# Kernel tuning notes

Measured on AMD Instinct MI355X. Metric: run time of the kernel, lower is better.

Reference implementation:

```python
import jax, jax.numpy as jnp
from jax import lax
import numpy as np

VOCAB, EMB, SEQ, HID, BATCH = 50000, 300, 80, 128, 4096


def setup_inputs() -> dict:
    key = jax.random.key(0)
    ks = jax.random.split(key, 7)
    x = jax.random.randint(ks[0], (BATCH, SEQ), 0, VOCAB)
    emb = jax.random.normal(ks[1], (VOCAB, EMB), jnp.float32) * 0.05  # frozen pretrained table
    # Keras SimpleRNN: kernel (glorot), recurrent_kernel (orthogonal-ish), bias zeros
    Wxh = jax.random.normal(ks[2], (EMB, HID), jnp.float32) * (1.0 / np.sqrt(EMB))
    Whh = jax.random.normal(ks[3], (HID, HID), jnp.float32) * (1.0 / np.sqrt(HID))
    bh = jnp.zeros((HID,), jnp.float32)
    Wd = jax.random.normal(ks[4], (HID, 1), jnp.float32) * (1.0 / np.sqrt(HID))
    bd = jnp.zeros((1,), jnp.float32)
    return {"x": x, "emb": emb, "Wxh": Wxh, "Whh": Whh, "bh": bh, "Wd": Wd, "bd": bd}


def reference(x, emb, Wxh, Whh, bh, Wd, bd):
    # Embedding lookup: [B, T] -> [B, T, E]
    e = emb[x]
    # Precompute input projection for all timesteps: [B, T, H]
    xp = jnp.einsum('bte,eh->bth', e, Wxh) + bh
    # SimpleRNN recurrence (tanh), return only last hidden state
    def step(h, xt):  # xt: [B, H]
        h = jnp.tanh(xt + h @ Whh)
        return h, None
    h0 = jnp.zeros((x.shape[0], Whh.shape[0]), xp.dtype)
    h_last, _ = lax.scan(step, h0, jnp.swapaxes(xp, 0, 1))  # scan over time
    # Dense(1, sigmoid): [B, 1]
    return jax.nn.sigmoid(h_last @ Wd + bd)
```

## Files before the change

### kernel.cpp

```cpp
#include <hip/hip_runtime.h>
#include <hip/hip_fp16.h>
#include <cstdint>

#define VOCAB 50000
#define EMB   300
#define SEQ   80
#define HID   128
#define BATCH 4096

typedef __attribute__((ext_vector_type(8))) _Float16 f16x8;
typedef __attribute__((ext_vector_type(4))) float    f32x4;

static __device__ __forceinline__ float fast_tanh(float xv) {
    const float e = __expf(2.f * xv);
    float r;
    asm("v_rcp_f32 %0, %1" : "=v"(r) : "v"(e + 1.f));
    return fmaf(-2.f, r, 1.f);
}
static __device__ __forceinline__ float f16b2f(unsigned short u) {
    _Float16 h; __builtin_memcpy(&h, &u, 2); return (float)h;
}
static __device__ __forceinline__ unsigned pack2h(float a, float b) {
    _Float16 ha = (_Float16)a, hb = (_Float16)b;
    unsigned short ua, ub;
    __builtin_memcpy(&ua, &ha, 2); __builtin_memcpy(&ub, &hb, 2);
    return (unsigned)ua | ((unsigned)ub << 16);
}

__global__ __launch_bounds__(256) void k_wprep(const float* __restrict__ Wxh,
                                               _Float16* __restrict__ W2) {
    const int c = blockIdx.x * 256 + threadIdx.x;
    if (c >= 5120) return;
    const int ks = c >> 9, rem = c & 511, col = rem >> 2, g = rem & 3;
    f16x8 f;
    #pragma unroll
    for (int j = 0; j < 8; ++j) {
        const int k = 32 * ks + 8 * g + j;
        f[j] = (_Float16)(k < EMB ? Wxh[k * HID + col] : 0.f);
    }
    *reinterpret_cast<f16x8*>(W2 + (size_t)c * 8) = f;
}

__global__ __launch_bounds__(256) void k_ptab(
    const float*    __restrict__ emb,
    const _Float16* __restrict__ W2,
    const float*    __restrict__ bh,
    _Float16*       __restrict__ P)
{
    __shared__ __align__(16) unsigned char Ps[16 * 256];

    const int tid = threadIdx.x, lane = tid & 63, wv = tid >> 6;
    const int r16 = lane & 15, g = lane >> 4;
    const int v0 = blockIdx.x * 64;

    f16x8 wa[10], wb[10];
    #pragma unroll
    for (int ks = 0; ks < 10; ++ks) {
        const int colA = 32 * wv + r16;
        wa[ks] = *reinterpret_cast<const f16x8*>(W2 + ((size_t)ks * 512 + colA * 4 + g) * 8);
        wb[ks] = *reinterpret_cast<const f16x8*>(W2 + ((size_t)ks * 512 + (colA + 16) * 4 + g) * 8);
    }
    const float4 bhA = *reinterpret_cast<const float4*>(bh + 32 * wv + 4 * g);
    const float4 bhB = *reinterpret_cast<const float4*>(bh + 32 * wv + 16 + 4 * g);

    const int psA = r16 * 256 + (((4 * wv + (g >> 1)) ^ r16) & 15) * 16 + (g & 1) * 8;
    const int psB = r16 * 256 + (((4 * wv + 2 + (g >> 1)) ^ r16) & 15) * 16 + (g & 1) * 8;
    const int srow = tid >> 4, schunk = tid & 15;
    const int sbyte = srow * 256 + ((schunk ^ srow) & 15) * 16;

    for (int tile = 0; tile < 4; ++tile) {
        const int row = v0 + tile * 16 + r16;
        const float* rp = emb + (size_t)min(row, VOCAB - 1) * EMB;

        f32x4 accA = {0.f, 0.f, 0.f, 0.f}, accB = {0.f, 0.f, 0.f, 0.f};
        #pragma unroll
        for (int ks = 0; ks < 9; ++ks) {
            const int c0 = 32 * ks + 8 * g;
            const float4 u0 = *reinterpret_cast<const float4*>(rp + c0);
            const float4 u1 = *reinterpret_cast<const float4*>(rp + c0 + 4);
            f16x8 ef;
            ef[0]=(_Float16)u0.x; ef[1]=(_Float16)u0.y; ef[2]=(_Float16)u0.z; ef[3]=(_Float16)u0.w;
            ef[4]=(_Float16)u1.x; ef[5]=(_Float16)u1.y; ef[6]=(_Float16)u1.z; ef[7]=(_Float16)u1.w;
            accA = __builtin_amdgcn_mfma_f32_16x16x32_f16(wa[ks], ef, accA, 0, 0, 0);
            accB = __builtin_amdgcn_mfma_f32_16x16x32_f16(wb[ks], ef, accB, 0, 0, 0);
        }
        {
            f16x8 ef;
            #pragma unroll
            for (int j = 0; j < 8; ++j) ef[j] = (_Float16)0.f;
            if (g == 0) {
                const float4 u0 = *reinterpret_cast<const float4*>(rp + 288);
                const float4 u1 = *reinterpret_cast<const float4*>(rp + 292);
                ef[0]=(_Float16)u0.x; ef[1]=(_Float16)u0.y; ef[2]=(_Float16)u0.z; ef[3]=(_Float16)u0.w;
                ef[4]=(_Float16)u1.x; ef[5]=(_Float16)u1.y; ef[6]=(_Float16)u1.z; ef[7]=(_Float16)u1.w;
            } else if (g == 1) {
                const float4 u0 = *reinterpret_cast<const float4*>(rp + 296);
                ef[0]=(_Float16)u0.x; ef[1]=(_Float16)u0.y; ef[2]=(_Float16)u0.z; ef[3]=(_Float16)u0.w;
            }
            accA = __builtin_amdgcn_mfma_f32_16x16x32_f16(wa[9], ef, accA, 0, 0, 0);
            accB = __builtin_amdgcn_mfma_f32_16x16x32_f16(wb[9], ef, accB, 0, 0, 0);
        }

        uint2 oA, oB;
        oA.x = pack2h(accA[0] + bhA.x, accA[1] + bhA.y);
        oA.y = pack2h(accA[2] + bhA.z, accA[3] + bhA.w);
        oB.x = pack2h(accB[0] + bhB.x, accB[1] + bhB.y);
        oB.y = pack2h(accB[2] + bhB.z, accB[3] + bhB.w);
        *reinterpret_cast<uint2*>(&Ps[psA]) = oA;
        *reinterpret_cast<uint2*>(&Ps[psB]) = oB;
        __syncthreads();

        const int orow = v0 + tile * 16 + srow;
        if (orow < VOCAB)
            *reinterpret_cast<uint4*>(P + (size_t)orow * HID + schunk * 8) =
                *reinterpret_cast<const uint4*>(&Ps[sbyte]);
        __syncthreads();
    }
}

__global__ __launch_bounds__(512, 2) void k_rnn(
    const int*      __restrict__ x,
    const _Float16* __restrict__ P,
    const float*    __restrict__ Whh,
    const float*    __restrict__ Wd,
    const float*    __restrict__ bd,
    float*          __restrict__ out)
{
    __shared__ __align__(16) unsigned char Xb[2][16 * 256];
    __shared__ __align__(16) unsigned char Hb[2][16 * 256];
    __shared__ int xidx[16 * SEQ];

    const int tid = threadIdx.x, lane = tid & 63, wv = tid >> 6;
    const int r16 = lane & 15, g = lane >> 4;
    const int rb = blockIdx.x * 16;

    for (int q = tid; q < 16 * SEQ; q += 512) xidx[q] = x[rb * SEQ + q];
    if (tid < 256) { uint4 z = {}; *reinterpret_cast<uint4*>(&Hb[0][tid * 16]) = z; }

    const int col = 16 * wv + r16;

    int h_rd[4];
    #pragma unroll
    for (int ks = 0; ks < 4; ++ks)
        h_rd[ks] = r16 * 256 + (((4 * ks + g) ^ r16) & 15) * 16;
    const int hw = r16 * 256 + (((2 * wv + (g >> 1)) ^ r16) & 15) * 16 + (g & 1) * 8;

    f16x8 wh[4];
    #pragma unroll
    for (int ks = 0; ks < 4; ++ks) {
        f16x8 f;
        #pragma unroll
        for (int j = 0; j < 8; ++j)
            f[j] = (_Float16)Whh[(32 * ks + 8 * g + j) * HID + col];
        wh[ks] = f;
    }

    const bool gon  = (tid < 256);
    const int  grow = (tid >> 4) & 15, gk = tid & 15;
    const int  gdst = grow * 256 + ((gk ^ grow) & 15) * 16;

    __syncthreads();

    if (gon)
        *reinterpret_cast<uint4*>(&Xb[0][gdst]) = *reinterpret_cast<const uint4*>(
            P + (size_t)xidx[grow * SEQ] * HID + 8 * gk);
    uint4 cur = {}, nxt = {};
    if (gon) cur = *reinterpret_cast<const uint4*>(
        P + (size_t)xidx[grow * SEQ + 1] * HID + 8 * gk);

    asm volatile("s_waitcnt lgkmcnt(0)" ::: "memory");
    __builtin_amdgcn_s_barrier();
    __builtin_amdgcn_sched_barrier(0);

#define STEP(T, PB, CUR, NXT)                                                      \
    {                                                                              \
        if ((T) + 1 < SEQ && gon)                                                  \
            *reinterpret_cast<uint4*>(&Xb[(PB) ^ 1][gdst]) = CUR;                  \
        if ((T) + 2 < SEQ && gon)                                                  \
            NXT = *reinterpret_cast<const uint4*>(                                 \
                P + (size_t)xidx[grow * SEQ + (T) + 2] * HID + 8 * gk);            \
        const uint2 xv = *reinterpret_cast<const uint2*>(&Xb[PB][hw]);             \
        f32x4 accA, accB = {0.f, 0.f, 0.f, 0.f};                                   \
        accA[0] = f16b2f((unsigned short)(xv.x & 0xffff));                         \
        accA[1] = f16b2f((unsigned short)(xv.x >> 16));                            \
        accA[2] = f16b2f((unsigned short)(xv.y & 0xffff));                         \
        accA[3] = f16b2f((unsigned short)(xv.y >> 16));                            \
        const f16x8 h0 = *reinterpret_cast<const f16x8*>(&Hb[PB][h_rd[0]]);        \
        const f16x8 h1 = *reinterpret_cast<const f16x8*>(&Hb[PB][h_rd[1]]);        \
        const f16x8 h2 = *reinterpret_cast<const f16x8*>(&Hb[PB][h_rd[2]]);        \
        const f16x8 h3 = *reinterpret_cast<const f16x8*>(&Hb[PB][h_rd[3]]);        \
        accA = __builtin_amdgcn_mfma_f32_16x16x32_f16(wh[0], h0, accA, 0, 0, 0);   \
        accB = __builtin_amdgcn_mfma_f32_16x16x32_f16(wh[1], h1, accB, 0, 0, 0);   \
        accA = __builtin_amdgcn_mfma_f32_16x16x32_f16(wh[2], h2, accA, 0, 0, 0);   \
        accB = __builtin_amdgcn_mfma_f32_16x16x32_f16(wh[3], h3, accB, 0, 0, 0);   \
        uint2 hv;                                                                  \
        hv.x = pack2h(fast_tanh(accA[0] + accB[0]), fast_tanh(accA[1] + accB[1])); \
        hv.y = pack2h(fast_tanh(accA[2] + accB[2]), fast_tanh(accA[3] + accB[3])); \
        *reinterpret_cast<uint2*>(&Hb[(PB) ^ 1][hw]) = hv;                         \
        asm volatile("s_waitcnt lgkmcnt(0)" ::: "memory");                         \
        __builtin_amdgcn_s_barrier();                                              \
        __builtin_amdgcn_sched_barrier(0);                                         \
    }

    for (int t = 0; t < SEQ; t += 2) {
        STEP(t,     0, cur, nxt);
        STEP(t + 1, 1, nxt, cur);
    }
#undef STEP

    const int r = tid >> 5, m = tid & 31;
    const int fb = r * 256 + (((m >> 1) ^ r) & 15) * 16 + (m & 1) * 8;
    const uint2 hv = *reinterpret_cast<const uint2*>(&Hb[0][fb]);
    const float4 wd = *reinterpret_cast<const float4*>(&Wd[4 * m]);
    float part = f16b2f((unsigned short)(hv.x & 0xffff)) * wd.x
               + f16b2f((unsigned short)(hv.x >> 16))    * wd.y
               + f16b2f((unsigned short)(hv.y & 0xffff)) * wd.z
               + f16b2f((unsigned short)(hv.y >> 16))    * wd.w;
    part += __shfl_down(part, 16, 32);
    part += __shfl_down(part, 8, 32);
    part += __shfl_down(part, 4, 32);
    part += __shfl_down(part, 2, 32);
    part += __shfl_down(part, 1, 32);
    if (m == 0) out[rb + r] = 1.f / (1.f + expf(-(part + bd[0])));
}

extern "C" void kernel_launch(void* const* d_in, const int* in_sizes, int n_in,
                              void* d_out, int out_size, void* d_ws, size_t ws_size,
                              hipStream_t stream)
{
    (void)in_sizes; (void)n_in; (void)out_size; (void)ws_size;
    const int*   x   = (const int*)  d_in[0];
    const float* emb = (const float*)d_in[1];
    const float* Wxh = (const float*)d_in[2];
    const float* Whh = (const float*)d_in[3];
    const float* bh  = (const float*)d_in[4];
    const float* Wd  = (const float*)d_in[5];
    const float* bd  = (const float*)d_in[6];
    float* out = (float*)d_out;

    _Float16* P  = (_Float16*)d_ws;
    _Float16* W2 = (_Float16*)((char*)d_ws + 12800000);

    k_wprep<<<20, 256, 0, stream>>>(Wxh, W2);
    k_ptab<<<(VOCAB + 63) / 64, 256, 0, stream>>>(emb, W2, bh, P);
    k_rnn<<<BATCH / 16, 512, 0, stream>>>(x, P, Whh, Wd, bd, out);
}
```

Measured before the change: 72.02 us.

## Halve RNN block rows, drop LDS x-staging, prefetch next embedding tile in ptab

The recurrence kernel now gives each 256-thread block 8 batch rows instead of 16, and each wave computes 32 hidden columns with two MFMA accumulators. This doubles the grid, aiming to fill more CUs and give each block shorter per-step work. The projected input is loaded straight from global memory into registers, one step ahead, instead of being staged through an LDS buffer. This removes the LDS write and read per step. The padded MFMA rows 8-15 duplicate row 7, so half the MFMA work is wasted. The projection-table kernel also software-pipelines its embedding-row loads one tile ahead, at the cost of more registers.

```diff
diff --git a/kernel.cpp b/kernel.cpp
--- a/kernel.cpp
+++ b/kernel.cpp
@@ -41,7 +41,7 @@
     *reinterpret_cast<f16x8*>(W2 + (size_t)c * 8) = f;
 }
 
-__global__ __launch_bounds__(256) void k_ptab(
+__global__ __launch_bounds__(256, 2) void k_ptab(
     const float*    __restrict__ emb,
     const _Float16* __restrict__ W2,
     const float*    __restrict__ bh,
@@ -68,37 +68,43 @@
     const int srow = tid >> 4, schunk = tid & 15;
     const int sbyte = srow * 256 + ((schunk ^ srow) & 15) * 16;
 
+    float4 u0[10], u1[10];
+
+#define LOADT(TILE)                                                               \
+    {                                                                             \
+        const float* rp = emb + (size_t)min(v0 + (TILE) * 16 + r16, VOCAB - 1) * EMB; \
+        _Pragma("unroll")                                                         \
+        for (int ks = 0; ks < 9; ++ks) {                                          \
+            u0[ks] = *reinterpret_cast<const float4*>(rp + 32 * ks + 8 * g);      \
+            u1[ks] = *reinterpret_cast<const float4*>(rp + 32 * ks + 8 * g + 4);  \
+        }                                                                         \
+        float4 z = {0.f, 0.f, 0.f, 0.f};                                          \
+        u0[9] = (g == 0) ? *reinterpret_cast<const float4*>(rp + 288)             \
+              : (g == 1) ? *reinterpret_cast<const float4*>(rp + 296) : z;        \
+        u1[9] = (g == 0) ? *reinterpret_cast<const float4*>(rp + 292) : z;        \
+    }
+
+    LOADT(0)
+
+    #pragma unroll
     for (int tile = 0; tile < 4; ++tile) {
-        const int row = v0 + tile * 16 + r16;
-        const float* rp = emb + (size_t)min(row, VOCAB - 1) * EMB;
+        f16x8 ef[10];
+        #pragma unroll
+        for (int ks = 0; ks < 10; ++ks) {
+            f16x8 f;
+            f[0] = (_Float16)u0[ks].x; f[1] = (_Float16)u0[ks].y;
+            f[2] = (_Float16)u0[ks].z; f[3] = (_Float16)u0[ks].w;
+            f[4] = (_Float16)u1[ks].x; f[5] = (_Float16)u1[ks].y;
+            f[6] = (_Float16)u1[ks].z; f[7] = (_Float16)u1[ks].w;
+            ef[ks] = f;
+        }
+        if (tile < 3) LOADT(tile + 1)
 
         f32x4 accA = {0.f, 0.f, 0.f, 0.f}, accB = {0.f, 0.f, 0.f, 0.f};
         #pragma unroll
-        for (int ks = 0; ks < 9; ++ks) {
-            const int c0 = 32 * ks + 8 * g;
-            const float4 u0 = *reinterpret_cast<const float4*>(rp + c0);
-            const float4 u1 = *reinterpret_cast<const float4*>(rp + c0 + 4);
-            f16x8 ef;
-            ef[0]=(_Float16)u0.x; ef[1]=(_Float16)u0.y; ef[2]=(_Float16)u0.z; ef[3]=(_Float16)u0.w;
-            ef[4]=(_Float16)u1.x; ef[5]=(_Float16)u1.y; ef[6]=(_Float16)u1.z; ef[7]=(_Float16)u1.w;
-            accA = __builtin_amdgcn_mfma_f32_16x16x32_f16(wa[ks], ef, accA, 0, 0, 0);
-            accB = __builtin_amdgcn_mfma_f32_16x16x32_f16(wb[ks], ef, accB, 0, 0, 0);
-        }
-        {
-            f16x8 ef;
-            #pragma unroll
-            for (int j = 0; j < 8; ++j) ef[j] = (_Float16)0.f;
-            if (g == 0) {
-                const float4 u0 = *reinterpret_cast<const float4*>(rp + 288);
-                const float4 u1 = *reinterpret_cast<const float4*>(rp + 292);
-                ef[0]=(_Float16)u0.x; ef[1]=(_Float16)u0.y; ef[2]=(_Float16)u0.z; ef[3]=(_Float16)u0.w;
-                ef[4]=(_Float16)u1.x; ef[5]=(_Float16)u1.y; ef[6]=(_Float16)u1.z; ef[7]=(_Float16)u1.w;
-            } else if (g == 1) {
-                const float4 u0 = *reinterpret_cast<const float4*>(rp + 296);
-                ef[0]=(_Float16)u0.x; ef[1]=(_Float16)u0.y; ef[2]=(_Float16)u0.z; ef[3]=(_Float16)u0.w;
-            }
-            accA = __builtin_amdgcn_mfma_f32_16x16x32_f16(wa[9], ef, accA, 0, 0, 0);
-            accB = __builtin_amdgcn_mfma_f32_16x16x32_f16(wb[9], ef, accB, 0, 0, 0);
+        for (int ks = 0; ks < 10; ++ks) {
+            accA = __builtin_amdgcn_mfma_f32_16x16x32_f16(wa[ks], ef[ks], accA, 0, 0, 0);
+            accB = __builtin_amdgcn_mfma_f32_16x16x32_f16(wb[ks], ef[ks], accB, 0, 0, 0);
         }
 
         uint2 oA, oB;
@@ -116,9 +122,10 @@
                 *reinterpret_cast<const uint4*>(&Ps[sbyte]);
         __syncthreads();
     }
-}
-
-__global__ __launch_bounds__(512, 2) void k_rnn(
+#undef LOADT
+}
+
+__global__ __launch_bounds__(256, 2) void k_rnn(
     const int*      __restrict__ x,
     const _Float16* __restrict__ P,
     const float*    __restrict__ Whh,
@@ -126,91 +133,107 @@
     const float*    __restrict__ bd,
     float*          __restrict__ out)
 {
-    __shared__ __align__(16) unsigned char Xb[2][16 * 256];
     __shared__ __align__(16) unsigned char Hb[2][16 * 256];
-    __shared__ int xidx[16 * SEQ];
+    __shared__ int xidx[8 * SEQ];
 
     const int tid = threadIdx.x, lane = tid & 63, wv = tid >> 6;
     const int r16 = lane & 15, g = lane >> 4;
-    const int rb = blockIdx.x * 16;
-
-    for (int q = tid; q < 16 * SEQ; q += 512) xidx[q] = x[rb * SEQ + q];
-    if (tid < 256) { uint4 z = {}; *reinterpret_cast<uint4*>(&Hb[0][tid * 16]) = z; }
-
-    const int col = 16 * wv + r16;
+    const int rb = blockIdx.x * 8;
+    const int r8 = min(r16, 7);
+
+    for (int q = tid; q < 8 * SEQ; q += 256) xidx[q] = x[rb * SEQ + q];
+    for (int q = tid; q < 512; q += 256) {
+        uint4 z = {};
+        *reinterpret_cast<uint4*>(&Hb[0][0] + 0) = z;
+        reinterpret_cast<uint4*>(&Hb[0][0])[q] = z;
+    }
+
+    const int cA = 32 * wv + 4 * g;
 
     int h_rd[4];
     #pragma unroll
     for (int ks = 0; ks < 4; ++ks)
         h_rd[ks] = r16 * 256 + (((4 * ks + g) ^ r16) & 15) * 16;
-    const int hw = r16 * 256 + (((2 * wv + (g >> 1)) ^ r16) & 15) * 16 + (g & 1) * 8;
-
-    f16x8 wh[4];
+    const int hw0 = r16 * 256 + (((4 * wv + (g >> 1)) ^ r16) & 15) * 16 + (g & 1) * 8;
+    const int hw1 = r16 * 256 + (((4 * wv + 2 + (g >> 1)) ^ r16) & 15) * 16 + (g & 1) * 8;
+
+    f16x8 wh0[4], wh1[4];
     #pragma unroll
     for (int ks = 0; ks < 4; ++ks) {
-        f16x8 f;
+        f16x8 f0, f1;
         #pragma unroll
-        for (int j = 0; j < 8; ++j)
-            f[j] = (_Float16)Whh[(32 * ks + 8 * g + j) * HID + col];
-        wh[ks] = f;
-    }
-
-    const bool gon  = (tid < 256);
-    const int  grow = (tid >> 4) & 15, gk = tid & 15;
-    const int  gdst = grow * 256 + ((gk ^ grow) & 15) * 16;
+        for (int j = 0; j < 8; ++j) {
+            const int k = 32 * ks + 8 * g + j;
+            f0[j] = (_Float16)Whh[k * HID + 32 * wv + r16];
+            f1[j] = (_Float16)Whh[k * HID + 32 * wv + 16 + r16];
+        }
+        wh0[ks] = f0; wh1[ks] = f1;
+    }
 
     __syncthreads();
 
-    if (gon)
-        *reinterpret_cast<uint4*>(&Xb[0][gdst]) = *reinterpret_cast<const uint4*>(
-            P + (size_t)xidx[grow * SEQ] * HID + 8 * gk);
-    uint4 cur = {}, nxt = {};
-    if (gon) cur = *reinterpret_cast<const uint4*>(
-        P + (size_t)xidx[grow * SEQ + 1] * HID + 8 * gk);
-
-    asm volatile("s_waitcnt lgkmcnt(0)" ::: "memory");
-    __builtin_amdgcn_s_barrier();
-    __builtin_amdgcn_sched_barrier(0);
-
-#define STEP(T, PB, CUR, NXT)                                                      \
+    uint2 xa0, xa1, xb0, xb1;
+    {
+        const _Float16* p0 = P + (size_t)xidx[r8 * SEQ + 0] * HID + cA;
+        xa0 = *reinterpret_cast<const uint2*>(p0);
+        xa1 = *reinterpret_cast<const uint2*>(p0 + 16);
+        const _Float16* p1 = P + (size_t)xidx[r8 * SEQ + 1] * HID + cA;
+        xb0 = *reinterpret_cast<const uint2*>(p1);
+        xb1 = *reinterpret_cast<const uint2*>(p1 + 16);
+    }
+
+#define STEP(T, PB, CA0, CA1)                                                      \
     {                                                                              \
-        if ((T) + 1 < SEQ && gon)                                                  \
-            *reinterpret_cast<uint4*>(&Xb[(PB) ^ 1][gdst]) = CUR;                  \
-        if ((T) + 2 < SEQ && gon)                                                  \
-            NXT = *reinterpret_cast<const uint4*>(                                 \
-                P + (size_t)xidx[grow * SEQ + (T) + 2] * HID + 8 * gk);            \
-        const uint2 xv = *reinterpret_cast<const uint2*>(&Xb[PB][hw]);             \
-        f32x4 accA, accB = {0.f, 0.f, 0.f, 0.f};                                   \
-        accA[0] = f16b2f((unsigned short)(xv.x & 0xffff));                         \
-        accA[1] = f16b2f((unsigned short)(xv.x >> 16));                            \
-        accA[2] = f16b2f((unsigned short)(xv.y & 0xffff));                         \
-        accA[3] = f16b2f((unsigned short)(xv.y >> 16));                            \
-        const f16x8 h0 = *reinterpret_cast<const f16x8*>(&Hb[PB][h_rd[0]]);        \
-        const f16x8 h1 = *reinterpret_cast<const f16x8*>(&Hb[PB][h_rd[1]]);        \
-        const f16x8 h2 = *reinterpret_cast<const f16x8*>(&Hb[PB][h_rd[2]]);        \
-        const f16x8 h3 = *reinterpret_cast<const f16x8*>(&Hb[PB][h_rd[3]]);        \
-        accA = __builtin_amdgcn_mfma_f32_16x16x32_f16(wh[0], h0, accA, 0, 0, 0);   \
-        accB = __builtin_amdgcn_mfma_f32_16x16x32_f16(wh[1], h1, accB, 0, 0, 0);   \
-        accA = __builtin_amdgcn_mfma_f32_16x16x32_f16(wh[2], h2, accA, 0, 0, 0);   \
-        accB = __builtin_amdgcn_mfma_f32_16x16x32_f16(wh[3], h3, accB, 0, 0, 0);   \
-        uint2 hv;                                                                  \
-        hv.x = pack2h(fast_tanh(accA[0] + accB[0]), fast_tanh(accA[1] + accB[1])); \
-        hv.y = pack2h(fast_tanh(accA[2] + accB[2]), fast_tanh(accA[3] + accB[3])); \
-        *reinterpret_cast<uint2*>(&Hb[(PB) ^ 1][hw]) = hv;                         \
+        f32x4 accA, accB;                                                          \
+        accA[0] = f16b2f((unsigned short)(CA0.x & 0xffff));                        \
+        accA[1] = f16b2f((unsigned short)(CA0.x >> 16));                           \
+        accA[2] = f16b2f((unsigned short)(CA0.y & 0xffff));                        \
+        accA[3] = f16b2f((unsigned short)(CA0.y >> 16));                           \
+        accB[0] = f16b2f((unsigned short)(CA1.x & 0xffff));                        \
+        accB[1] = f16b2f((unsigned short)(CA1.x >> 16));                           \
+        accB[2] = f16b2f((unsigned short)(CA1.y & 0xffff));                        \
+        accB[3] = f16b2f((unsigned short)(CA1.y >> 16));                           \
+        if ((T) + 2 < SEQ) {                 \
+            const _Float16* np = P + (size_t)xidx[r8 * SEQ + (T) + 2] * HID + cA;  \
+            CA0 = *reinterpret_cast<const uint2*>(np);                             \
+            CA1 = *reinterpret_cast<const uint2*>(np + 16);                        \
+        }                                                                          \
+        const unsigned char* hb = &Hb[PB][0];                                      \
+        const f16x8 h0 = *reinterpret_cast<const f16x8*>(hb + h_rd[0]);            \
+        const f16x8 h1 = *reinterpret_cast<const f16x8*>(hb + h_rd[1]);            \
+        const f16x8 h2 = *reinterpret_cast<const f16x8*>(hb + h_rd[2]);            \
+        const f16x8 h3 = *reinterpret_cast<const f16x8*>(hb + h_rd[3]);            \
+        accA = __builtin_amdgcn_mfma_f32_16x16x32_f16(wh0[0], h0, accA, 0, 0, 0);  \
+        accB = __builtin_amdgcn_mfma_f32_16x16x32_f16(wh1[0], h0, accB, 0, 0, 0);  \
+        accA = __builtin_amdgcn_mfma_f32_16x16x32_f16(wh0[1], h1, accA, 0, 0, 0);  \
+        accB = __builtin_amdgcn_mfma_f32_16x16x32_f16(wh1[1], h1, accB, 0, 0, 0);  \
+        accA = __builtin_amdgcn_mfma_f32_16x16x32_f16(wh0[2], h2, accA, 0, 0, 0);  \
+        accB = __builtin_amdgcn_mfma_f32_16x16x32_f16(wh1[2], h2, accB, 0, 0, 0);  \
+        accA = __builtin_amdgcn_mfma_f32_16x16x32_f16(wh0[3], h3, accA, 0, 0, 0);  \
+        accB = __builtin_amdgcn_mfma_f32_16x16x32_f16(wh1[3], h3, accB, 0, 0, 0);  \
+        unsigned char* hwp = &Hb[(PB) ^ 1][0];                                     \
+        uint2 o0, o1;                                                              \
+        o0.x = pack2h(fast_tanh(accA[0]), fast_tanh(accA[1]));                     \
+        o0.y = pack2h(fast_tanh(accA[2]), fast_tanh(accA[3]));                     \
+        o1.x = pack2h(fast_tanh(accB[0]), fast_tanh(accB[1]));                     \
+        o1.y = pack2h(fast_tanh(accB[2]), fast_tanh(accB[3]));                     \
+        *reinterpret_cast<uint2*>(hwp + hw0) = o0;                                 \
+        *reinterpret_cast<uint2*>(hwp + hw1) = o1;                                 \
         asm volatile("s_waitcnt lgkmcnt(0)" ::: "memory");                         \
         __builtin_amdgcn_s_barrier();                                              \
         __builtin_amdgcn_sched_barrier(0);                                         \
     }
 
     for (int t = 0; t < SEQ; t += 2) {
-        STEP(t,     0, cur, nxt);
-        STEP(t + 1, 1, nxt, cur);
+        STEP(t,     0, xa0, xa1);
+        STEP(t + 1, 1, xb0, xb1);
     }
 #undef STEP
 
+    const char* hb0 = (const char*)&Hb[0][0];
     const int r = tid >> 5, m = tid & 31;
     const int fb = r * 256 + (((m >> 1) ^ r) & 15) * 16 + (m & 1) * 8;
-    const uint2 hv = *reinterpret_cast<const uint2*>(&Hb[0][fb]);
+    const uint2 hv = *reinterpret_cast<const uint2*>(hb0 + fb);
     const float4 wd = *reinterpret_cast<const float4*>(&Wd[4 * m]);
     float part = f16b2f((unsigned short)(hv.x & 0xffff)) * wd.x
                + f16b2f((unsigned short)(hv.x >> 16))    * wd.y
@@ -243,5 +266,5 @@
 
     k_wprep<<<20, 256, 0, stream>>>(Wxh, W2);
     k_ptab<<<(VOCAB + 63) / 64, 256, 0, stream>>>(emb, W2, bh, P);
-    k_rnn<<<BATCH / 16, 512, 0, stream>>>(x, P, Whh, Wd, bd, out);
-}
+    k_rnn<<<BATCH / 8, 256, 0, stream>>>(x, P, Whh, Wd, bd, out);
+}
```

After: 83.99 us. 1.17x slower.

## Run each RNN batch tile in a single wavefront, removing block barriers

Applied to the files above, without the earlier changes.

The recurrence kernel now gives each 16-row batch tile to one 64-lane wavefront. That wavefront holds all of Whh, pre-swizzled by the prep kernel, in registers and computes all 128 hidden columns with 32 MFMAs per step, so the per-step block barrier is gone. The hidden state is exchanged through LDS within the wave only, and the next x-projection rows are gathered straight into registers two steps ahead. The projection-table kernel also changes: each wave handles its own 16 vocab rows, keeps the embedding fragments in registers, streams weight columns through double-buffered registers and writes directly without LDS staging. In exchange, fewer waves run per CU (256 single-wave blocks) and register pressure is high, so parallelism and latency hiding may suffer.

```diff
diff --git a/kernel.cpp b/kernel.cpp
--- a/kernel.cpp
+++ b/kernel.cpp
@@ -28,200 +28,227 @@
 }
 
 __global__ __launch_bounds__(256) void k_wprep(const float* __restrict__ Wxh,
-                                               _Float16* __restrict__ W2) {
+                                               const float* __restrict__ Whh,
+                                               _Float16* __restrict__ W2,
+                                               _Float16* __restrict__ W3) {
     const int c = blockIdx.x * 256 + threadIdx.x;
-    if (c >= 5120) return;
-    const int ks = c >> 9, rem = c & 511, col = rem >> 2, g = rem & 3;
-    f16x8 f;
-    #pragma unroll
-    for (int j = 0; j < 8; ++j) {
-        const int k = 32 * ks + 8 * g + j;
-        f[j] = (_Float16)(k < EMB ? Wxh[k * HID + col] : 0.f);
-    }
-    *reinterpret_cast<f16x8*>(W2 + (size_t)c * 8) = f;
-}
-
-__global__ __launch_bounds__(256) void k_ptab(
+    if (c < 5120) {
+        const int ks = c >> 9, rem = c & 511, col = rem >> 2, g = rem & 3;
+        f16x8 f;
+        #pragma unroll
+        for (int j = 0; j < 8; ++j) {
+            const int k = 32 * ks + 8 * g + j;
+            f[j] = (_Float16)(k < EMB ? Wxh[k * HID + col] : 0.f);
+        }
+        *reinterpret_cast<f16x8*>(W2 + (size_t)c * 8) = f;
+    } else if (c < 7168) {
+        const int c2 = c - 5120;
+        const int ct = c2 >> 8, ks = (c2 >> 6) & 3, l = c2 & 63;
+        const int g = l >> 4, r16 = l & 15;
+        f16x8 f;
+        #pragma unroll
+        for (int j = 0; j < 8; ++j)
+            f[j] = (_Float16)Whh[(32 * ks + 8 * g + j) * HID + 16 * ct + r16];
+        *reinterpret_cast<f16x8*>(W3 + (size_t)c2 * 8) = f;
+    }
+}
+
+__global__ __launch_bounds__(256, 2) void k_ptab(
     const float*    __restrict__ emb,
     const _Float16* __restrict__ W2,
     const float*    __restrict__ bh,
     _Float16*       __restrict__ P)
 {
-    __shared__ __align__(16) unsigned char Ps[16 * 256];
-
     const int tid = threadIdx.x, lane = tid & 63, wv = tid >> 6;
     const int r16 = lane & 15, g = lane >> 4;
-    const int v0 = blockIdx.x * 64;
-
-    f16x8 wa[10], wb[10];
-    #pragma unroll
-    for (int ks = 0; ks < 10; ++ks) {
-        const int colA = 32 * wv + r16;
-        wa[ks] = *reinterpret_cast<const f16x8*>(W2 + ((size_t)ks * 512 + colA * 4 + g) * 8);
-        wb[ks] = *reinterpret_cast<const f16x8*>(W2 + ((size_t)ks * 512 + (colA + 16) * 4 + g) * 8);
-    }
-    const float4 bhA = *reinterpret_cast<const float4*>(bh + 32 * wv + 4 * g);
-    const float4 bhB = *reinterpret_cast<const float4*>(bh + 32 * wv + 16 + 4 * g);
-
-    const int psA = r16 * 256 + (((4 * wv + (g >> 1)) ^ r16) & 15) * 16 + (g & 1) * 8;
-    const int psB = r16 * 256 + (((4 * wv + 2 + (g >> 1)) ^ r16) & 15) * 16 + (g & 1) * 8;
-    const int srow = tid >> 4, schunk = tid & 15;
-    const int sbyte = srow * 256 + ((schunk ^ srow) & 15) * 16;
-
-    for (int tile = 0; tile < 4; ++tile) {
-        const int row = v0 + tile * 16 + r16;
-        const float* rp = emb + (size_t)min(row, VOCAB - 1) * EMB;
-
-        f32x4 accA = {0.f, 0.f, 0.f, 0.f}, accB = {0.f, 0.f, 0.f, 0.f};
-        #pragma unroll
-        for (int ks = 0; ks < 9; ++ks) {
-            const int c0 = 32 * ks + 8 * g;
-            const float4 u0 = *reinterpret_cast<const float4*>(rp + c0);
-            const float4 u1 = *reinterpret_cast<const float4*>(rp + c0 + 4);
-            f16x8 ef;
-            ef[0]=(_Float16)u0.x; ef[1]=(_Float16)u0.y; ef[2]=(_Float16)u0.z; ef[3]=(_Float16)u0.w;
-            ef[4]=(_Float16)u1.x; ef[5]=(_Float16)u1.y; ef[6]=(_Float16)u1.z; ef[7]=(_Float16)u1.w;
-            accA = __builtin_amdgcn_mfma_f32_16x16x32_f16(wa[ks], ef, accA, 0, 0, 0);
-            accB = __builtin_amdgcn_mfma_f32_16x16x32_f16(wb[ks], ef, accB, 0, 0, 0);
-        }
-        {
-            f16x8 ef;
+    const int row = blockIdx.x * 64 + wv * 16 + r16;
+    const float* rp = emb + (size_t)(row < VOCAB ? row : VOCAB - 1) * EMB;
+    const bool wr = (row < VOCAB);
+
+    f16x8 ef[10];
+    #pragma unroll
+    for (int ks = 0; ks < 9; ++ks) {
+        const float4 u0 = *reinterpret_cast<const float4*>(rp + 32 * ks + 8 * g);
+        const float4 u1 = *reinterpret_cast<const float4*>(rp + 32 * ks + 8 * g + 4);
+        f16x8 f;
+        f[0] = (_Float16)u0.x; f[1] = (_Float16)u0.y;
+        f[2] = (_Float16)u0.z; f[3] = (_Float16)u0.w;
+        f[4] = (_Float16)u1.x; f[5] = (_Float16)u1.y;
+        f[6] = (_Float16)u1.z; f[7] = (_Float16)u1.w;
+        ef[ks] = f;
+    }
+    {
+        f16x8 f;
+        #pragma unroll
+        for (int j = 0; j < 8; ++j) f[j] = (_Float16)0.f;
+        if (g == 0) {
+            const float4 u0 = *reinterpret_cast<const float4*>(rp + 288);
+            const float4 u1 = *reinterpret_cast<const float4*>(rp + 292);
+            f[0] = (_Float16)u0.x; f[1] = (_Float16)u0.y;
+            f[2] = (_Float16)u0.z; f[3] = (_Float16)u0.w;
+            f[4] = (_Float16)u1.x; f[5] = (_Float16)u1.y;
+            f[6] = (_Float16)u1.z; f[7] = (_Float16)u1.w;
+        } else if (g == 1) {
+            const float4 u0 = *reinterpret_cast<const float4*>(rp + 296);
+            f[0] = (_Float16)u0.x; f[1] = (_Float16)u0.y;
+            f[2] = (_Float16)u0.z; f[3] = (_Float16)u0.w;
+        }
+        ef[9] = f;
+    }
+
+    float4 bhf[8];
+    #pragma unroll
+    for (int ct = 0; ct < 8; ++ct)
+        bhf[ct] = *reinterpret_cast<const float4*>(bh + 16 * ct + 4 * g);
+
+    f16x8 wA[10], wB[10];
+    #pragma unroll
+    for (int ks = 0; ks < 10; ++ks)
+        wA[ks] = *reinterpret_cast<const f16x8*>(
+            W2 + ((size_t)ks * 512 + (size_t)r16 * 4 + g) * 8);
+
+    char* const po = (char*)(P + (size_t)(wr ? row : 0) * HID);
+
+    #pragma unroll
+    for (int ct = 0; ct < 8; ++ct) {
+        if (ct < 7) {
+            const int coln = 16 * (ct + 1) + r16;
             #pragma unroll
-            for (int j = 0; j < 8; ++j) ef[j] = (_Float16)0.f;
-            if (g == 0) {
-                const float4 u0 = *reinterpret_cast<const float4*>(rp + 288);
-                const float4 u1 = *reinterpret_cast<const float4*>(rp + 292);
-                ef[0]=(_Float16)u0.x; ef[1]=(_Float16)u0.y; ef[2]=(_Float16)u0.z; ef[3]=(_Float16)u0.w;
-                ef[4]=(_Float16)u1.x; ef[5]=(_Float16)u1.y; ef[6]=(_Float16)u1.z; ef[7]=(_Float16)u1.w;
-            } else if (g == 1) {
-                const float4 u0 = *reinterpret_cast<const float4*>(rp + 296);
-                ef[0]=(_Float16)u0.x; ef[1]=(_Float16)u0.y; ef[2]=(_Float16)u0.z; ef[3]=(_Float16)u0.w;
-            }
-            accA = __builtin_amdgcn_mfma_f32_16x16x32_f16(wa[9], ef, accA, 0, 0, 0);
-            accB = __builtin_amdgcn_mfma_f32_16x16x32_f16(wb[9], ef, accB, 0, 0, 0);
-        }
-
-        uint2 oA, oB;
-        oA.x = pack2h(accA[0] + bhA.x, accA[1] + bhA.y);
-        oA.y = pack2h(accA[2] + bhA.z, accA[3] + bhA.w);
-        oB.x = pack2h(accB[0] + bhB.x, accB[1] + bhB.y);
-        oB.y = pack2h(accB[2] + bhB.z, accB[3] + bhB.w);
-        *reinterpret_cast<uint2*>(&Ps[psA]) = oA;
-        *reinterpret_cast<uint2*>(&Ps[psB]) = oB;
-        __syncthreads();
-
-        const int orow = v0 + tile * 16 + srow;
-        if (orow < VOCAB)
-            *reinterpret_cast<uint4*>(P + (size_t)orow * HID + schunk * 8) =
-                *reinterpret_cast<const uint4*>(&Ps[sbyte]);
-        __syncthreads();
-    }
-}
-
-__global__ __launch_bounds__(512, 2) void k_rnn(
+            for (int ks = 0; ks < 10; ++ks)
+                ((ct & 1) ? wA : wB)[ks] = *reinterpret_cast<const f16x8*>(
+                    W2 + ((size_t)ks * 512 + (size_t)coln * 4 + g) * 8);
+        }
+        const f16x8* wc = (ct & 1) ? wB : wA;
+        f32x4 a0 = {0.f, 0.f, 0.f, 0.f}, a1 = {0.f, 0.f, 0.f, 0.f};
+        #pragma unroll
+        for (int ks = 0; ks < 10; ks += 2) {
+            a0 = __builtin_amdgcn_mfma_f32_16x16x32_f16(wc[ks],     ef[ks],     a0, 0, 0, 0);
+            a1 = __builtin_amdgcn_mfma_f32_16x16x32_f16(wc[ks + 1], ef[ks + 1], a1, 0, 0, 0);
+        }
+        uint2 o;
+        o.x = pack2h(a0[0] + a1[0] + bhf[ct].x, a0[1] + a1[1] + bhf[ct].y);
+        o.y = pack2h(a0[2] + a1[2] + bhf[ct].z, a0[3] + a1[3] + bhf[ct].w);
+        if (wr) *reinterpret_cast<uint2*>(po + 32 * ct + 8 * g) = o;
+    }
+}
+
+__global__ __launch_bounds__(64, 1) void k_rnn(
     const int*      __restrict__ x,
     const _Float16* __restrict__ P,
-    const float*    __restrict__ Whh,
+    const _Float16* __restrict__ W3,
     const float*    __restrict__ Wd,
     const float*    __restrict__ bd,
     float*          __restrict__ out)
 {
-    __shared__ __align__(16) unsigned char Xb[2][16 * 256];
-    __shared__ __align__(16) unsigned char Hb[2][16 * 256];
+    __shared__ __align__(16) unsigned char Hx[16 * 256];
     __shared__ int xidx[16 * SEQ];
 
-    const int tid = threadIdx.x, lane = tid & 63, wv = tid >> 6;
+    const int lane = threadIdx.x;
     const int r16 = lane & 15, g = lane >> 4;
     const int rb = blockIdx.x * 16;
 
-    for (int q = tid; q < 16 * SEQ; q += 512) xidx[q] = x[rb * SEQ + q];
-    if (tid < 256) { uint4 z = {}; *reinterpret_cast<uint4*>(&Hb[0][tid * 16]) = z; }
-
-    const int col = 16 * wv + r16;
-
-    int h_rd[4];
+    for (int q = lane; q < 16 * SEQ; q += 64) xidx[q] = x[rb * SEQ + q];
+
+    f16x8 wh[8][4];
+    #pragma unroll
+    for (int ct = 0; ct < 8; ++ct)
+        #pragma unroll
+        for (int ks = 0; ks < 4; ++ks)
+            wh[ct][ks] = *reinterpret_cast<const f16x8*>(
+                W3 + ((size_t)(ct * 4 + ks) * 64 + lane) * 8);
+
+    int wr_off[8], rd_off[4];
+    #pragma unroll
+    for (int ct = 0; ct < 8; ++ct)
+        wr_off[ct] = r16 * 256 + (((2 * ct + (g >> 1)) ^ r16) & 15) * 16 + (g & 1) * 8;
     #pragma unroll
     for (int ks = 0; ks < 4; ++ks)
-        h_rd[ks] = r16 * 256 + (((4 * ks + g) ^ r16) & 15) * 16;
-    const int hw = r16 * 256 + (((2 * wv + (g >> 1)) ^ r16) & 15) * 16 + (g & 1) * 8;
-
-    f16x8 wh[4];
-    #pragma unroll
-    for (int ks = 0; ks < 4; ++ks) {
-        f16x8 f;
-        #pragma unroll
-        for (int j = 0; j < 8; ++j)
-            f[j] = (_Float16)Whh[(32 * ks + 8 * g + j) * HID + col];
-        wh[ks] = f;
-    }
-
-    const bool gon  = (tid < 256);
-    const int  grow = (tid >> 4) & 15, gk = tid & 15;
-    const int  gdst = grow * 256 + ((gk ^ grow) & 15) * 16;
-
-    __syncthreads();
-
-    if (gon)
-        *reinterpret_cast<uint4*>(&Xb[0][gdst]) = *reinterpret_cast<const uint4*>(
-            P + (size_t)xidx[grow * SEQ] * HID + 8 * gk);
-    uint4 cur = {}, nxt = {};
-    if (gon) cur = *reinterpret_cast<const uint4*>(
-        P + (size_t)xidx[grow * SEQ + 1] * HID + 8 * gk);
-
-    asm volatile("s_waitcnt lgkmcnt(0)" ::: "memory");
-    __builtin_amdgcn_s_barrier();
-    __builtin_amdgcn_sched_barrier(0);
-
-#define STEP(T, PB, CUR, NXT)                                                      \
-    {                                                                              \
-        if ((T) + 1 < SEQ && gon)                                                  \
-            *reinterpret_cast<uint4*>(&Xb[(PB) ^ 1][gdst]) = CUR;                  \
-        if ((T) + 2 < SEQ && gon)                                                  \
-            NXT = *reinterpret_cast<const uint4*>(                                 \
-                P + (size_t)xidx[grow * SEQ + (T) + 2] * HID + 8 * gk);            \
-        const uint2 xv = *reinterpret_cast<const uint2*>(&Xb[PB][hw]);             \
-        f32x4 accA, accB = {0.f, 0.f, 0.f, 0.f};                                   \
-        accA[0] = f16b2f((unsigned short)(xv.x & 0xffff));                         \
-        accA[1] = f16b2f((unsigned short)(xv.x >> 16));                            \
-        accA[2] = f16b2f((unsigned short)(xv.y & 0xffff));                         \
-        accA[3] = f16b2f((unsigned short)(xv.y >> 16));                            \
-        const f16x8 h0 = *reinterpret_cast<const f16x8*>(&Hb[PB][h_rd[0]]);        \
-        const f16x8 h1 = *reinterpret_cast<const f16x8*>(&Hb[PB][h_rd[1]]);        \
-        const f16x8 h2 = *reinterpret_cast<const f16x8*>(&Hb[PB][h_rd[2]]);        \
-        const f16x8 h3 = *reinterpret_cast<const f16x8*>(&Hb[PB][h_rd[3]]);        \
-        accA = __builtin_amdgcn_mfma_f32_16x16x32_f16(wh[0], h0, accA, 0, 0, 0);   \
-        accB = __builtin_amdgcn_mfma_f32_16x16x32_f16(wh[1], h1, accB, 0, 0, 0);   \
-        accA = __builtin_amdgcn_mfma_f32_16x16x32_f16(wh[2], h2, accA, 0, 0, 0);   \
-        accB = __builtin_amdgcn_mfma_f32_16x16x32_f16(wh[3], h3, accB, 0, 0, 0);   \
-        uint2 hv;                                                                  \
-        hv.x = pack2h(fast_tanh(accA[0] + accB[0]), fast_tanh(accA[1] + accB[1])); \
-        hv.y = pack2h(fast_tanh(accA[2] + accB[2]), fast_tanh(accA[3] + accB[3])); \
-        *reinterpret_cast<uint2*>(&Hb[(PB) ^ 1][hw]) = hv;                         \
-        asm volatile("s_waitcnt lgkmcnt(0)" ::: "memory");                         \
-        __builtin_amdgcn_s_barrier();                                              \
-        __builtin_amdgcn_sched_barrier(0);                                         \
-    }
-
-    for (int t = 0; t < SEQ; t += 2) {
-        STEP(t,     0, cur, nxt);
-        STEP(t + 1, 1, nxt, cur);
-    }
-#undef STEP
-
-    const int r = tid >> 5, m = tid & 31;
-    const int fb = r * 256 + (((m >> 1) ^ r) & 15) * 16 + (m & 1) * 8;
-    const uint2 hv = *reinterpret_cast<const uint2*>(&Hb[0][fb]);
-    const float4 wd = *reinterpret_cast<const float4*>(&Wd[4 * m]);
-    float part = f16b2f((unsigned short)(hv.x & 0xffff)) * wd.x
-               + f16b2f((unsigned short)(hv.x >> 16))    * wd.y
-               + f16b2f((unsigned short)(hv.y & 0xffff)) * wd.z
-               + f16b2f((unsigned short)(hv.y >> 16))    * wd.w;
-    part += __shfl_down(part, 16, 32);
-    part += __shfl_down(part, 8, 32);
-    part += __shfl_down(part, 4, 32);
-    part += __shfl_down(part, 2, 32);
-    part += __shfl_down(part, 1, 32);
-    if (m == 0) out[rb + r] = 1.f / (1.f + expf(-(part + bd[0])));
+        rd_off[ks] = r16 * 256 + (((4 * ks + g) ^ r16) & 15) * 16;
+
+    f16x8 hf[4];
+    {
+        f16x8 hz;
+        #pragma unroll
+        for (int j = 0; j < 8; ++j) hz[j] = (_Float16)0.f;
+        hf[0] = hz; hf[1] = hz; hf[2] = hz; hf[3] = hz;
+    }
+    uint2 xc[8], xn[8];
+    {
+        const int i0 = xidx[r16 * SEQ + 0];
+        const int i1 = xidx[r16 * SEQ + 1];
+        const char* p0 = (const char*)P + (size_t)i0 * 256 + g * 8;
+        const char* p1 = (const char*)P + (size_t)i1 * 256 + g * 8;
+        #pragma unroll
+        for (int ct = 0; ct < 8; ++ct) {
+            xc[ct] = *reinterpret_cast<const uint2*>(p0 + ct * 32);
+            xn[ct] = *reinterpret_cast<const uint2*>(p1 + ct * 32);
+        }
+    }
+
+    f32x4 acc[8], th[8];
+
+#define RNN_STEP(TT, XC, DO_GATHER, DO_EXCH)                                   \
+    {                                                                          \
+        _Pragma("unroll")                                                      \
+        for (int ct = 0; ct < 8; ++ct) {                                       \
+            acc[ct][0] = f16b2f((unsigned short)(XC[ct].x & 0xffff));          \
+            acc[ct][1] = f16b2f((unsigned short)(XC[ct].x >> 16));             \
+            acc[ct][2] = f16b2f((unsigned short)(XC[ct].y & 0xffff));          \
+            acc[ct][3] = f16b2f((unsigned short)(XC[ct].y >> 16));             \
+        }                                                                      \
+        if (DO_GATHER) {       \
+            const int idx2 = xidx[r16 * SEQ + (TT) + 2];                       \
+            const char* pp = (const char*)P + (size_t)idx2 * 256 + g * 8;      \
+            _Pragma("unroll")                                                  \
+            for (int ct = 0; ct < 8; ++ct)                                     \
+                XC[ct] = *reinterpret_cast<const uint2*>(pp + ct * 32);        \
+        }                                                                      \
+        _Pragma("unroll")                                                      \
+        for (int ks = 0; ks < 4; ++ks)                                         \
+            _Pragma("unroll")                                                  \
+            for (int ct = 0; ct < 8; ++ct)                                     \
+                acc[ct] = __builtin_amdgcn_mfma_f32_16x16x32_f16(              \
+                    wh[ct][ks], hf[ks], acc[ct], 0, 0, 0);                     \
+        _Pragma("unroll")                                                      \
+        for (int ct = 0; ct < 8; ++ct) {                                       \
+            th[ct][0] = fast_tanh(acc[ct][0]);                                 \
+            th[ct][1] = fast_tanh(acc[ct][1]);                                 \
+            th[ct][2] = fast_tanh(acc[ct][2]);                                 \
+            th[ct][3] = fast_tanh(acc[ct][3]);                                 \
+        }                                                                      \
+        if (DO_EXCH) {                                                         \
+            _Pragma("unroll")                                                  \
+            for (int ct = 0; ct < 8; ++ct) {                                   \
+                uint2 o;                                                       \
+                o.x = pack2h(th[ct][0], th[ct][1]);                            \
+                o.y = pack2h(th[ct][2], th[ct][3]);                            \
+                *reinterpret_cast<uint2*>(Hx + wr_off[ct]) = o;                \
+            }                                                                  \
+            _Pragma("unroll")                                                  \
+            for (int ks = 0; ks < 4; ++ks)                                     \
+                hf[ks] = *reinterpret_cast<const f16x8*>(Hx + rd_off[ks]);     \
+        }                                                                      \
+    }
+
+    #pragma unroll 1
+    for (int t = 0; t < SEQ - 3; t += 2) {
+        RNN_STEP(t,     xc, true, true);
+        RNN_STEP(t + 1, xn, true, true);
+    }
+    RNN_STEP(78, xc, false, true);
+    RNN_STEP(79, xn, false, false);
+#undef RNN_STEP
+
+    float part = 0.f;
+    #pragma unroll
+    for (int ct = 0; ct < 8; ++ct) {
+        const float4 wd = *reinterpret_cast<const float4*>(Wd + 16 * ct + 4 * g);
+        part += th[ct][0] * wd.x + th[ct][1] * wd.y
+              + th[ct][2] * wd.z + th[ct][3] * wd.w;
+    }
+    part += __shfl_xor(part, 16, 64);
+    part += __shfl_xor(part, 32, 64);
+    if (lane < 16) out[rb + r16] = 1.f / (1.f + expf(-(part + bd[0])));
 }
 
 extern "C" void kernel_launch(void* const* d_in, const int* in_sizes, int n_in,
@@ -240,8 +267,9 @@
 
     _Float16* P  = (_Float16*)d_ws;
     _Float16* W2 = (_Float16*)((char*)d_ws + 12800000);
-
-    k_wprep<<<20, 256, 0, stream>>>(Wxh, W2);
+    _Float16* W3 = (_Float16*)((char*)d_ws + 12881920);
+
+    k_wprep<<<28, 256, 0, stream>>>(Wxh, Whh, W2, W3);
     k_ptab<<<(VOCAB + 63) / 64, 256, 0, stream>>>(emb, W2, bh, P);
-    k_rnn<<<BATCH / 16, 512, 0, stream>>>(x, P, Whh, Wd, bd, out);
-}
+    k_rnn<<<BATCH / 16, 64, 0, stream>>>(x, P, W3, Wd, bd, out);
+}
```

New measurement: 119.5 us. 1.66x slower.
